# Kernel optimization log

Hardware: AMD Instinct MI355X
Metric: run time of the kernel (lower is better)

## Reference

```python
import jax, jax.numpy as jnp
import numpy as np

B, L, F, E, D, N_OUT, FC = 2048, 100, 64, 256, 256, 3, 128


def _lstm_cell(x, h, c, Wi, Wh, b):
    gates = x @ Wi + h @ Wh + b  # (B, 4H)
    i, f, g, o = jnp.split(gates, 4, axis=-1)
    c_new = jax.nn.sigmoid(f) * c + jax.nn.sigmoid(i) * jnp.tanh(g)
    h_new = jax.nn.sigmoid(o) * jnp.tanh(c_new)
    return h_new, c_new


def setup_inputs() -> dict:
    key = jax.random.key(0)
    ks = jax.random.split(key, 12)
    s = 0.05
    return {
        "x": jax.random.normal(ks[0], (B, L, F), jnp.float32),
        # encoder input-attention (shared across timesteps, as in [layer]*look_back)
        "Wa": jax.random.normal(ks[1], (F + E, F), jnp.float32) * s,
        "ba": jnp.zeros((F,), jnp.float32),
        # encoder LSTM cell
        "Wi": jax.random.normal(ks[2], (F, 4 * E), jnp.float32) * s,
        "Wh": jax.random.normal(ks[3], (E, 4 * E), jnp.float32) * s,
        "be": jnp.zeros((4 * E,), jnp.float32),
        # decoder temporal attention
        "Wd": jax.random.normal(ks[4], (E + D, D), jnp.float32) * s,
        "bd": jnp.zeros((D,), jnp.float32),
        "Wl": jax.random.normal(ks[5], (D, 1), jnp.float32) * s,
        "bl": jnp.zeros((1,), jnp.float32),
        # decoder LSTM cell
        "Wdi": jax.random.normal(ks[6], (E, 4 * D), jnp.float32) * s,
        "Wdh": jax.random.normal(ks[7], (D, 4 * D), jnp.float32) * s,
        "bdec": jnp.zeros((4 * D,), jnp.float32),
        # output head: tanh(D->FC) then tanh(FC->1)
        "Wf": jax.random.normal(ks[8], (D, FC), jnp.float32) * s,
        "bf": jnp.zeros((FC,), jnp.float32),
        "Wo": jax.random.normal(ks[9], (FC, 1), jnp.float32) * s,
        "bo": jnp.zeros((1,), jnp.float32),
    }


def reference(x, Wa, ba, Wi, Wh, be, Wd, bd, Wl, bl, Wdi, Wdh, bdec, Wf, bf, Wo, bo):
    # ---------- encoder: per-timestep input attention + LSTM cell ----------
    x_t = jnp.transpose(x, (1, 0, 2))  # (L, B, F)

    def enc_step(carry, xt):
        h, c = carry
        energies = jnp.tanh(jnp.concatenate([xt, h], axis=1) @ Wa + ba)  # (B, F)
        a = jax.nn.softmax(energies, axis=1)
        enc_in = a * xt  # attended input (B, F)
        h, c = _lstm_cell(enc_in, h, c, Wi, Wh, be)
        return (h, c), h

    h0 = jnp.zeros((B, E), x.dtype)
    c0 = jnp.zeros((B, E), x.dtype)
    _, enc_out = jax.lax.scan(enc_step, (h0, c0), x_t)  # (L, B, E)

    # ---------- decoder: temporal attention over encoder states + LSTM ----------
    h_d = jnp.zeros((B, D), x.dtype)
    c_d = jnp.zeros((B, D), x.dtype)
    outs = []
    for _ in range(N_OUT):  # small fixed output horizon
        con = jnp.broadcast_to(h_d[None, :, :], (L, B, D))
        en = jnp.tanh(jnp.concatenate([enc_out, con], axis=2) @ Wd + bd)  # (L, B, D)
        scores = en @ Wl + bl  # (L, B, 1)
        alpha = jax.nn.softmax(scores, axis=0)  # over time
        ctx = jnp.sum(alpha * enc_out, axis=0)  # (B, E)
        h_d, c_d = _lstm_cell(ctx, h_d, c_d, Wdi, Wdh, bdec)
        fc = jnp.tanh(h_d @ Wf + bf)  # (B, FC)
        outs.append(jnp.tanh(fc @ Wo + bo))  # (B, 1)
    return jnp.concatenate(outs, axis=1)  # (B, n_output)
```

## Files before the change

### kernel.cpp

```cpp
#include <hip/hip_runtime.h>
#include <math.h>

#define BB 2048
#define LL 100
#define FF 64
#define EE 256
#define DD 256
#define NOUT 3

#define COMP(v, i) ((i) == 0 ? (v).x : (i) == 1 ? (v).y : (i) == 2 ? (v).z : (v).w)

typedef unsigned short u16;
typedef unsigned int u32;
typedef __attribute__((ext_vector_type(8))) __bf16 bf16x8;
typedef __attribute__((ext_vector_type(4))) float f32x4;
typedef __attribute__((ext_vector_type(2))) float f32x2;

#define MFMA_(A, B, C) __builtin_amdgcn_mfma_f32_16x16x32_bf16((A), (B), (C), 0, 0, 0)

__device__ __forceinline__ float sigmoidf_(float x) {
    return 1.0f / (1.0f + expf(-x));
}
__device__ __forceinline__ float tanhf_(float x) {
    return 1.0f - 2.0f / (1.0f + expf(2.0f * x));
}
__device__ __forceinline__ u16 f2b_(float f) {
    u32 u = __float_as_uint(f);
    u = (u + 0x7FFFu + ((u >> 16) & 1u)) >> 16;
    return (u16)u;
}
__device__ __forceinline__ float b2f_(u16 b) {
    return __uint_as_float(((u32)b) << 16);
}
__device__ __forceinline__ u32 pack2_(float a, float b) {
    return (u32)f2b_(a) | ((u32)f2b_(b) << 16);
}
__device__ __forceinline__ f32x4 splat4(float b) {
    f32x4 v; v[0] = b; v[1] = b; v[2] = b; v[3] = b; return v;
}
__device__ __forceinline__ void split8(const float* v, uint4& H, uint4& L) {
    u16 h[8], lo[8];
    #pragma unroll
    for (int e = 0; e < 8; ++e) {
        h[e]  = f2b_(v[e]);
        lo[e] = f2b_(v[e] - b2f_(h[e]));
    }
    H = make_uint4((u32)h[0]  | ((u32)h[1]  << 16), (u32)h[2]  | ((u32)h[3]  << 16),
                   (u32)h[4]  | ((u32)h[5]  << 16), (u32)h[6]  | ((u32)h[7]  << 16));
    L = make_uint4((u32)lo[0] | ((u32)lo[1] << 16), (u32)lo[2] | ((u32)lo[3] << 16),
                   (u32)lo[4] | ((u32)lo[5] << 16), (u32)lo[6] | ((u32)lo[7] << 16));
}

#define AF(mt, kt, p, ln) (((((mt) * 10 + (kt)) * 2 + (p)) * 64 + (ln)) * 8)
#define AFX(mt, kt, p, ln) AF(mt, kt, p, (ln) ^ (((ln) >> 4) & 3))
#define AF2(mt, kt, p, ln) (((((mt) * 8 + (kt)) * 2 + (p)) * 64 + (ln)) * 8)

__global__ __launch_bounds__(64) void w_prep_all(
    const float* __restrict__ Wi, const float* __restrict__ Wh,
    const float* __restrict__ Wa, const float* __restrict__ Wd,
    u16* __restrict__ wp)
{
    const int bid = blockIdx.x;
    const int l   = threadIdx.x;

    float v[8];
    if (bid < 640) {
        const int nt = bid / 10, kt = bid - nt * 10;
        const int col = nt * 16 + (l & 15);
        #pragma unroll
        for (int e = 0; e < 8; ++e) {
            const int k = kt * 32 + ((l >> 4) << 3) + e;
            v[e] = (k < 64) ? Wi[(size_t)k * 1024 + col]
                            : Wh[(size_t)(k - 64) * 1024 + col];
        }
    } else if (bid < 680) {
        const int b2 = bid - 640;
        const int nt = b2 / 10, kt = b2 - nt * 10;
        const int col = nt * 16 + (l & 15);
        #pragma unroll
        for (int e = 0; e < 8; ++e) {
            const int k = kt * 32 + ((l >> 4) << 3) + e;
            v[e] = Wa[(size_t)k * 64 + col];
        }
    } else {
        const int b2 = bid - 680;
        const int nt = b2 >> 3, kt = b2 & 7;
        const int col = nt * 16 + (l & 15);
        #pragma unroll
        for (int e = 0; e < 8; ++e) {
            const int k = kt * 32 + ((l >> 4) << 3) + e;
            v[e] = Wd[(size_t)k * 256 + col];
        }
    }
    uint4 H, L;
    split8(v, H, L);
    *(uint4*)&wp[(size_t)bid * 1024 + (size_t)l * 8]       = H;
    *(uint4*)&wp[(size_t)bid * 1024 + 512 + (size_t)l * 8] = L;
}

__global__ __launch_bounds__(1024) void enc_mfma4(
    const float* __restrict__ x,
    const float* __restrict__ ba, const float* __restrict__ be,
    const u16* __restrict__ wp,
    float* __restrict__ enc_out,
    float* __restrict__ hbuf,
    u32* __restrict__ flags)
{
    __shared__ u16   aFrag[20480];
    __shared__ float x_s[32 * 68];
    __shared__ float e_s[32 * 68];
    __shared__ float gate_s[4][32][66];

    const int bid = blockIdx.x;
    const int g   = (bid & 7) | ((bid >> 5) << 3);
    const int p   = (bid >> 3) & 3;
    const int row0 = g * 32;
    const int tid = threadIdx.x;
    const int l   = tid & 63;
    const int w   = tid >> 6;

    for (int v = tid; v < 20480 / 2; v += 1024) ((u32*)aFrag)[v] = 0u;

    const int ntW = (w >> 2) * 16 + p * 4 + (w & 3);
    uint4 BhR[10];
    #pragma unroll
    for (int kt = 0; kt < 10; ++kt)
        BhR[kt] = *(const uint4*)&wp[(size_t)(ntW * 10 + kt) * 1024 + (size_t)l * 8];

    const float be_r = be[(size_t)ntW * 16 + (l & 15)];
    const float ba_r = (w < 8) ? ba[(w & 3) * 16 + (l & 15)] : 0.f;

    float c_state[2] = {0.f, 0.f};

    __syncthreads();

    for (int t = 0; t < LL; ++t) {
        if (t > 0) {
            if (tid == 0) {
                const u32 target = 4u * (u32)t;
                int guard = 0;
                while (__hip_atomic_load(&flags[g * 32], __ATOMIC_RELAXED,
                                         __HIP_MEMORY_SCOPE_AGENT) < target) {
                    __builtin_amdgcn_s_sleep(1);
                    if (++guard > 2000000) break;
                }
            }
            __syncthreads();
        }

        if (tid < 256) {
            const int kt2 = tid >> 7;
            const int mt  = (tid >> 6) & 1;
            const int l2  = tid & 63;
            const int row2 = mt * 16 + (l2 & 15);
            const int f0   = kt2 * 32 + ((l2 >> 4) << 3);
            const float* xp = x + (size_t)(row0 + row2) * (LL * FF) + (size_t)t * FF + f0;
            float4 xa = *(const float4*)xp;
            float4 xb = *(const float4*)(xp + 4);
            float v[8] = {xa.x, xa.y, xa.z, xa.w, xb.x, xb.y, xb.z, xb.w};
            uint4 H, L;
            split8(v, H, L);
            *(uint4*)&aFrag[AFX(mt, kt2, 0, l2)] = H;
            *(uint4*)&aFrag[AFX(mt, kt2, 1, l2)] = L;
            *(float4*)&x_s[row2 * 68 + f0]     = xa;
            *(float4*)&x_s[row2 * 68 + f0 + 4] = xb;
        } else if (t > 0) {
            const int v   = tid - 256;
            const int prl = v >> 8;
            const int vv  = v & 255;
            const int row = vv >> 3;
            const int i8  = vv & 7;
            const int ugp = (p + 1 + prl) & 3;
            const int u8  = ugp * 64 + i8 * 8;
            const float* hp_g = hbuf + ((size_t)((t - 1) & 1) * BB + row0 + row) * 256 + u8;
            f32x4 a4, b4;
            asm volatile("global_load_dwordx4 %0, %2, off sc0 sc1\n\t"
                         "global_load_dwordx4 %1, %3, off sc0 sc1\n\t"
                         "s_waitcnt vmcnt(0)"
                         : "=v"(a4), "=v"(b4)
                         : "v"(hp_g), "v"(hp_g + 4) : "memory");
            float v8[8] = {a4[0], a4[1], a4[2], a4[3], b4[0], b4[1], b4[2], b4[3]};
            uint4 H, L;
            split8(v8, H, L);
            const int mt = row >> 4, rowT = row & 15;
            const int kt_h = 2 + (u8 >> 5);
            const int g2   = (u8 & 31) >> 3;
            const int ln   = rowT + (g2 << 4);
            *(uint4*)&aFrag[AFX(mt, kt_h, 0, ln)] = H;
            *(uint4*)&aFrag[AFX(mt, kt_h, 1, ln)] = L;
        }
        __syncthreads();

        if (w < 8) {
            const int mt  = w >> 2;
            const int nta = w & 3;
            f32x4 ea = splat4(ba_r);
            #pragma unroll
            for (int kt = 0; kt < 10; ++kt) {
                bf16x8 Ah = *(const bf16x8*)&aFrag[AFX(mt, kt, 0, l)];
                bf16x8 Al = *(const bf16x8*)&aFrag[AFX(mt, kt, 1, l)];
                const size_t o = (size_t)(640 + nta * 10 + kt) * 1024 + (size_t)l * 8;
                bf16x8 Bh = *(const bf16x8*)&wp[o];
                bf16x8 Bl = *(const bf16x8*)&wp[o + 512];
                ea = MFMA_(Ah, Bh, ea);
                ea = MFMA_(Al, Bh, ea);
                ea = MFMA_(Ah, Bl, ea);
            }
            const int colA = nta * 16 + (l & 15);
            #pragma unroll
            for (int r = 0; r < 4; ++r) {
                const int rowT = ((l >> 4) << 2) + r;
                e_s[(mt * 16 + rowT) * 68 + colA] = tanhf_(ea[r]);
            }
        }
        __syncthreads();

        if (tid < 512) {
            const int row2 = tid >> 4;
            const int c4   = (tid & 15) * 4;
            float4 ev = *(const float4*)&e_s[row2 * 68 + c4];
            float m = fmaxf(fmaxf(ev.x, ev.y), fmaxf(ev.z, ev.w));
            #pragma unroll
            for (int msk = 8; msk >= 1; msk >>= 1) m = fmaxf(m, __shfl_xor(m, msk, 64));
            float4 ex;
            ex.x = expf(ev.x - m); ex.y = expf(ev.y - m);
            ex.z = expf(ev.z - m); ex.w = expf(ev.w - m);
            float s = ex.x + ex.y + ex.z + ex.w;
            #pragma unroll
            for (int msk = 8; msk >= 1; msk >>= 1) s += __shfl_xor(s, msk, 64);
            const float inv = 1.f / s;
            float4 xv = *(const float4*)&x_s[row2 * 68 + c4];
            float ein[4] = { ex.x * inv * xv.x, ex.y * inv * xv.y,
                             ex.z * inv * xv.z, ex.w * inv * xv.w };
            const int mt   = row2 >> 4;
            const int rowT = row2 & 15;
            const int kt   = c4 >> 5;
            const int g2   = (c4 & 31) >> 3;
            const int e0   = c4 & 7;
            const int ln   = rowT + (g2 << 4);
            ushort4 h4, l4;
            #pragma unroll
            for (int e = 0; e < 4; ++e) {
                u16 hh = f2b_(ein[e]);
                u16 ll = f2b_(ein[e] - b2f_(hh));
                if (e == 0) { h4.x = hh; l4.x = ll; } else if (e == 1) { h4.y = hh; l4.y = ll; }
                else if (e == 2) { h4.z = hh; l4.z = ll; } else { h4.w = hh; l4.w = ll; }
            }
            *(ushort4*)&aFrag[AFX(mt, kt, 0, ln) + e0] = h4;
            *(ushort4*)&aFrag[AFX(mt, kt, 1, ln) + e0] = l4;
        }
        __syncthreads();

        f32x4 acc0 = splat4(be_r), acc1 = splat4(be_r);
        #pragma unroll
        for (int kt = 0; kt < 10; ++kt) {
            bf16x8 Ah0 = *(const bf16x8*)&aFrag[AFX(0, kt, 0, l)];
            bf16x8 Al0 = *(const bf16x8*)&aFrag[AFX(0, kt, 1, l)];
            bf16x8 Ah1 = *(const bf16x8*)&aFrag[AFX(1, kt, 0, l)];
            bf16x8 Al1 = *(const bf16x8*)&aFrag[AFX(1, kt, 1, l)];
            bf16x8 Bl  = *(const bf16x8*)&wp[(size_t)(ntW * 10 + kt) * 1024 + 512 + (size_t)l * 8];
            bf16x8 Bh  = __builtin_bit_cast(bf16x8, BhR[kt]);
            acc0 = MFMA_(Ah0, Bh, acc0);
            acc1 = MFMA_(Ah1, Bh, acc1);
            acc0 = MFMA_(Al0, Bh, acc0);
            acc1 = MFMA_(Al1, Bh, acc1);
            acc0 = MFMA_(Ah0, Bl, acc0);
            acc1 = MFMA_(Ah1, Bl, acc1);
        }
        {
            const int gate = w >> 2;
            const int ulb  = (w & 3) * 16 + (l & 15);
            #pragma unroll
            for (int r = 0; r < 4; ++r) {
                const int rT = ((l >> 4) << 2) + r;
                gate_s[gate][rT][ulb]      = acc0[r];
                gate_s[gate][16 + rT][ulb] = acc1[r];
            }
        }
        __syncthreads();

        {
            const int row = tid >> 5;
            const int q2  = (tid & 31) * 2;
            float gi0 = gate_s[0][row][q2], gi1 = gate_s[0][row][q2 + 1];
            float gf0 = gate_s[1][row][q2], gf1 = gate_s[1][row][q2 + 1];
            float gg0 = gate_s[2][row][q2], gg1 = gate_s[2][row][q2 + 1];
            float go0 = gate_s[3][row][q2], go1 = gate_s[3][row][q2 + 1];
            float cv0 = sigmoidf_(gf0) * c_state[0] + sigmoidf_(gi0) * tanhf_(gg0);
            float cv1 = sigmoidf_(gf1) * c_state[1] + sigmoidf_(gi1) * tanhf_(gg1);
            c_state[0] = cv0; c_state[1] = cv1;
            float hv0 = sigmoidf_(go0) * tanhf_(cv0);
            float hv1 = sigmoidf_(go1) * tanhf_(cv1);
            const int u_g = p * 64 + q2;
            *(float2*)&enc_out[((size_t)t * BB + row0 + row) * 256 + u_g]
                = make_float2(hv0, hv1);
            float* hp_g = hbuf + ((size_t)(t & 1) * BB + row0 + row) * 256 + u_g;
            f32x2 hv2; hv2[0] = hv0; hv2[1] = hv1;
            asm volatile("global_store_dwordx2 %0, %1, off sc0 sc1"
                         :: "v"(hp_g), "v"(hv2) : "memory");
            const int mt = row >> 4, rowT = row & 15;
            const int kt_h = 2 + (u_g >> 5);
            const int g2   = (u_g & 31) >> 3;
            const int ln   = rowT + (g2 << 4);
            const int e    = u_g & 7;
            ((u32*)aFrag)[(AFX(mt, kt_h, 0, ln) + e) >> 1] = pack2_(hv0, hv1);
            u16 h0 = f2b_(hv0), h1 = f2b_(hv1);
            ((u32*)aFrag)[(AFX(mt, kt_h, 1, ln) + e) >> 1] =
                (u32)f2b_(hv0 - b2f_(h0)) | ((u32)f2b_(hv1 - b2f_(h1)) << 16);
        }
        asm volatile("s_waitcnt vmcnt(0)" ::: "memory");
        __syncthreads();
        if (tid == 0)
            __hip_atomic_fetch_add(&flags[g * 32], 1u, __ATOMIC_RELEASE,
                                   __HIP_MEMORY_SCOPE_AGENT);
    }
}

__global__ __launch_bounds__(256) void gemm_ep_mfma(
    const float* __restrict__ A, const u16* __restrict__ wp,
    float* __restrict__ C)
{
    __shared__ u16   aF[2 * 8 * 2 * 64 * 8];
    __shared__ float c_s[32 * 260];
    const int m0  = blockIdx.x * 32;
    const int tid = threadIdx.x;
    const int l   = tid & 63;
    const int w   = tid >> 6;

    for (int s = tid; s < 1024; s += 256) {
        const int mt = s >> 9, kt = (s >> 6) & 7, l2 = s & 63;
        const int row2 = mt * 16 + (l2 & 15);
        const int k0   = kt * 32 + ((l2 >> 4) << 3);
        const float* ap = A + (size_t)(m0 + row2) * 256 + k0;
        float4 xa = *(const float4*)ap;
        float4 xb = *(const float4*)(ap + 4);
        float v[8] = {xa.x, xa.y, xa.z, xa.w, xb.x, xb.y, xb.z, xb.w};
        uint4 H, L;
        split8(v, H, L);
        *(uint4*)&aF[AF2(mt, kt, 0, l2)] = H;
        *(uint4*)&aF[AF2(mt, kt, 1, l2)] = L;
    }
    __syncthreads();

    f32x4 acc[2][4];
    #pragma unroll
    for (int mt = 0; mt < 2; ++mt)
        #pragma unroll
        for (int j = 0; j < 4; ++j) acc[mt][j] = splat4(0.f);

    #pragma unroll
    for (int kt = 0; kt < 8; ++kt) {
        bf16x8 Ah0 = *(const bf16x8*)&aF[AF2(0, kt, 0, l)];
        bf16x8 Al0 = *(const bf16x8*)&aF[AF2(0, kt, 1, l)];
        bf16x8 Ah1 = *(const bf16x8*)&aF[AF2(1, kt, 0, l)];
        bf16x8 Al1 = *(const bf16x8*)&aF[AF2(1, kt, 1, l)];
        #pragma unroll
        for (int j = 0; j < 4; ++j) {
            const int nt = w * 4 + j;
            const u16* bt = wp + (size_t)(680 + nt * 8 + kt) * 1024 + (size_t)l * 8;
            bf16x8 Bh = *(const bf16x8*)bt;
            bf16x8 Bl = *(const bf16x8*)(bt + 512);
            acc[0][j] = MFMA_(Ah0, Bh, acc[0][j]);
            acc[1][j] = MFMA_(Ah1, Bh, acc[1][j]);
            acc[0][j] = MFMA_(Al0, Bh, acc[0][j]);
            acc[1][j] = MFMA_(Al1, Bh, acc[1][j]);
            acc[0][j] = MFMA_(Ah0, Bl, acc[0][j]);
            acc[1][j] = MFMA_(Ah1, Bl, acc[1][j]);
        }
    }

    #pragma unroll
    for (int mt = 0; mt < 2; ++mt)
        #pragma unroll
        for (int j = 0; j < 4; ++j) {
            const int col = (w * 4 + j) * 16 + (l & 15);
            #pragma unroll
            for (int r = 0; r < 4; ++r) {
                const int row = mt * 16 + ((l >> 4) << 2) + r;
                c_s[row * 260 + col] = acc[mt][j][r];
            }
        }
    __syncthreads();
    for (int v = tid; v < 32 * 64; v += 256) {
        const int row = v >> 6, c4 = (v & 63) << 2;
        *(float4*)&C[(size_t)(m0 + row) * 256 + c4] = *(const float4*)&c_s[row * 260 + c4];
    }
}

__global__ __launch_bounds__(256) void gemm_nk256(
    const float* __restrict__ A, const float* __restrict__ W,
    const float* __restrict__ bias, float* __restrict__ C, int skip_gemm)
{
    __shared__ float a_s[32 * 256];
    const int m0   = blockIdx.x * 32;
    const int tid  = threadIdx.x;
    const int lane = tid & 63;
    const int rg   = tid >> 6;
    const int n0   = lane * 4;

    float4 bias4 = make_float4(0.f, 0.f, 0.f, 0.f);
    if (bias) bias4 = *(const float4*)&bias[n0];

    if (skip_gemm) {
        #pragma unroll
        for (int r = 0; r < 8; ++r)
            *(float4*)&C[(size_t)(m0 + rg * 8 + r) * 256 + n0] = bias4;
        return;
    }

    for (int v = tid; v < 32 * 64; v += 256)
        ((float4*)a_s)[v] = ((const float4*)(A + (size_t)m0 * 256))[v];
    __syncthreads();

    float4 acc[8];
    #pragma unroll
    for (int r = 0; r < 8; ++r) acc[r] = bias4;

    #pragma unroll 2
    for (int k = 0; k < 256; k += 4) {
        float4 wv[4];
        #pragma unroll
        for (int kk = 0; kk < 4; ++kk)
            wv[kk] = *(const float4*)&W[(size_t)(k + kk) * 256 + n0];
        float4 av[8];
        #pragma unroll
        for (int r = 0; r < 8; ++r)
            av[r] = *(const float4*)&a_s[(rg * 8 + r) * 256 + k];
        #pragma unroll
        for (int kk = 0; kk < 4; ++kk) {
            #pragma unroll
            for (int r = 0; r < 8; ++r) {
                float e = COMP(av[r], kk);
                acc[r].x += e * wv[kk].x; acc[r].y += e * wv[kk].y;
                acc[r].z += e * wv[kk].z; acc[r].w += e * wv[kk].w;
            }
        }
    }
    #pragma unroll
    for (int r = 0; r < 8; ++r)
        *(float4*)&C[(size_t)(m0 + rg * 8 + r) * 256 + n0] = acc[r];
}

__global__ __launch_bounds__(256) void pack_ep(
    float* A, const float* __restrict__ W, u16* epOut, int packed)
{
    __shared__ float a_s[32 * 256];
    const int m0   = blockIdx.x * 32;
    const int tid  = threadIdx.x;
    const int lane = tid & 63;
    const int rg   = tid >> 6;
    const int n0   = lane * 4;

    for (int v = tid; v < 32 * 64; v += 256)
        ((float4*)a_s)[v] = ((const float4*)(A + (size_t)m0 * 256))[v];
    __syncthreads();

    float4 acc[8];
    #pragma unroll
    for (int r = 0; r < 8; ++r) acc[r] = make_float4(0.f, 0.f, 0.f, 0.f);

    #pragma unroll 2
    for (int k = 0; k < 256; k += 4) {
        float4 wv[4];
        #pragma unroll
        for (int kk = 0; kk < 4; ++kk)
            wv[kk] = *(const float4*)&W[(size_t)(k + kk) * 256 + n0];
        float4 av[8];
        #pragma unroll
        for (int r = 0; r < 8; ++r)
            av[r] = *(const float4*)&a_s[(rg * 8 + r) * 256 + k];
        #pragma unroll
        for (int kk = 0; kk < 4; ++kk) {
            #pragma unroll
            for (int r = 0; r < 8; ++r) {
                float e = COMP(av[r], kk);
                acc[r].x += e * wv[kk].x; acc[r].y += e * wv[kk].y;
                acc[r].z += e * wv[kk].z; acc[r].w += e * wv[kk].w;
            }
        }
    }

    u16* epu = packed ? (u16*)A : epOut;
    #pragma unroll
    for (int r = 0; r < 8; ++r) {
        const size_t row = (size_t)(m0 + rg * 8 + r);
        ushort4 o;
        o.x = f2b_(acc[r].x); o.y = f2b_(acc[r].y);
        o.z = f2b_(acc[r].z); o.w = f2b_(acc[r].w);
        u16* dst = packed ? (epu + row * 512 + 256 + n0)
                          : (epu + row * 256 + n0);
        *(ushort4*)dst = o;
    }

    if (packed) {
        u32* ab = (u32*)A;
        for (int v = tid; v < 32 * 128; v += 256) {
            const int row = v >> 7, j = v & 127;
            float2 f = *(const float2*)&a_s[(row << 8) + (j << 1)];
            ab[((size_t)(m0 + row)) * 256 + j] = pack2_(f.x, f.y);
        }
    }
}

__global__ __launch_bounds__(256) void scores_ep_f32(
    const float* __restrict__ ep, const float* __restrict__ hp,
    const float* __restrict__ Wl, float* __restrict__ scores)
{
    __shared__ float hp_s[8 * 256];
    const int b0  = blockIdx.x * 8;
    const int l0  = blockIdx.y * 20;
    const int tid = threadIdx.x;
    const int r   = tid >> 5;
    const int g   = tid & 31;

    for (int v = tid; v < 512; v += 256)
        ((float4*)hp_s)[v] = ((const float4*)(hp + (size_t)b0 * 256))[v];
    __syncthreads();

    const float4 wl0 = *(const float4*)&Wl[g * 4];
    const float4 wl1 = *(const float4*)&Wl[128 + g * 4];
    const float4 h0  = *(const float4*)&hp_s[r * 256 + g * 4];
    const float4 h1  = *(const float4*)&hp_s[r * 256 + 128 + g * 4];
    const float* eb  = ep + (size_t)l0 * (BB * 256) + (size_t)(b0 + r) * 256;

    #pragma unroll 2
    for (int li = 0; li < 20; ++li) {
        float4 e0 = *(const float4*)&eb[(size_t)li * (BB * 256) + g * 4];
        float4 e1 = *(const float4*)&eb[(size_t)li * (BB * 256) + 128 + g * 4];
        float p = tanhf_(e0.x + h0.x) * wl0.x + tanhf_(e0.y + h0.y) * wl0.y
                + tanhf_(e0.z + h0.z) * wl0.z + tanhf_(e0.w + h0.w) * wl0.w
                + tanhf_(e1.x + h1.x) * wl1.x + tanhf_(e1.y + h1.y) * wl1.y
                + tanhf_(e1.z + h1.z) * wl1.z + tanhf_(e1.w + h1.w) * wl1.w;
        #pragma unroll
        for (int msk = 16; msk >= 1; msk >>= 1) p += __shfl_xor(p, msk, 64);
        if (g == 0) scores[(size_t)(l0 + li) * BB + b0 + r] = p;
    }
}

__global__ __launch_bounds__(256) void scores_ep_b16(
    const u16* __restrict__ ep, const float* __restrict__ hp,
    const float* __restrict__ Wl, float* __restrict__ scores,
    int sstr, int soff)
{
    __shared__ float hp_s[8 * 256];
    const int b0  = blockIdx.x * 8;
    const int l0  = blockIdx.y * 20;
    const int tid = threadIdx.x;
    const int r   = tid >> 5;
    const int g   = tid & 31;

    for (int v = tid; v < 512; v += 256)
        ((float4*)hp_s)[v] = ((const float4*)(hp + (size_t)b0 * 256))[v];
    __syncthreads();

    const float4 wl0 = *(const float4*)&Wl[g * 4];
    const float4 wl1 = *(const float4*)&Wl[128 + g * 4];
    const float4 h0  = *(const float4*)&hp_s[r * 256 + g * 4];
    const float4 h1  = *(const float4*)&hp_s[r * 256 + 128 + g * 4];

    #pragma unroll 2
    for (int li = 0; li < 20; ++li) {
        const u16* er = ep + ((size_t)(l0 + li) * BB + b0 + r) * sstr + soff;
        ushort4 u0 = *(const ushort4*)&er[g * 4];
        ushort4 u1 = *(const ushort4*)&er[128 + g * 4];
        float p = tanhf_(b2f_(u0.x) + h0.x) * wl0.x + tanhf_(b2f_(u0.y) + h0.y) * wl0.y
                + tanhf_(b2f_(u0.z) + h0.z) * wl0.z + tanhf_(b2f_(u0.w) + h0.w) * wl0.w
                + tanhf_(b2f_(u1.x) + h1.x) * wl1.x + tanhf_(b2f_(u1.y) + h1.y) * wl1.y
                + tanhf_(b2f_(u1.z) + h1.z) * wl1.z + tanhf_(b2f_(u1.w) + h1.w) * wl1.w;
        #pragma unroll
        for (int msk = 16; msk >= 1; msk >>= 1) p += __shfl_xor(p, msk, 64);
        if (g == 0) scores[(size_t)(l0 + li) * BB + b0 + r] = p;
    }
}

__global__ __launch_bounds__(256) void softmax_ctx(
    const float* __restrict__ scores, const float* __restrict__ enc_out,
    float* __restrict__ ctx)
{
    __shared__ float al_s[8 * 100];
    const int b0  = blockIdx.x * 8;
    const int tid = threadIdx.x;
    for (int v = tid; v < 800; v += 256) {
        int r = v / 100, l = v - r * 100;
        al_s[r * 100 + l] = scores[(size_t)l * BB + b0 + r];
    }
    __syncthreads();
    if (tid < 8) {
        float m = -1e30f;
        for (int l = 0; l < LL; ++l) m = fmaxf(m, al_s[tid * 100 + l]);
        float s = 0.f;
        for (int l = 0; l < LL; ++l) { float e = expf(al_s[tid * 100 + l] - m); al_s[tid * 100 + l] = e; s += e; }
        float inv = 1.f / s;
        for (int l = 0; l < LL; ++l) al_s[tid * 100 + l] *= inv;
    }
    __syncthreads();
    float acc[8] = {};
    for (int l = 0; l < LL; ++l) {
        const float* er = enc_out + (size_t)l * (BB * 256) + (size_t)b0 * 256 + tid;
        #pragma unroll
        for (int r = 0; r < 8; ++r) acc[r] += al_s[r * 100 + l] * er[r * 256];
    }
    for (int r = 0; r < 8; ++r) ctx[(size_t)(b0 + r) * 256 + tid] = acc[r];
}

__global__ __launch_bounds__(256) void softmax_ctx_b16(
    const float* __restrict__ scores, const u16* __restrict__ encp,
    float* __restrict__ ctx)
{
    __shared__ float al_s[8 * 100];
    const int b0  = blockIdx.x * 8;
    const int tid = threadIdx.x;
    for (int v = tid; v < 800; v += 256) {
        int r = v / 100, l = v - r * 100;
        al_s[r * 100 + l] = scores[(size_t)l * BB + b0 + r];
    }
    __syncthreads();
    if (tid < 8) {
        float m = -1e30f;
        for (int l = 0; l < LL; ++l) m = fmaxf(m, al_s[tid * 100 + l]);
        float s = 0.f;
        for (int l = 0; l < LL; ++l) { float e = expf(al_s[tid * 100 + l] - m); al_s[tid * 100 + l] = e; s += e; }
        float inv = 1.f / s;
        for (int l = 0; l < LL; ++l) al_s[tid * 100 + l] *= inv;
    }
    __syncthreads();
    float acc[8] = {};
    for (int l = 0; l < LL; ++l) {
        const u16* er = encp + ((size_t)l * BB + b0) * 512 + tid;
        #pragma unroll
        for (int r = 0; r < 8; ++r) acc[r] += al_s[r * 100 + l] * b2f_(er[r * 512]);
    }
    for (int r = 0; r < 8; ++r) ctx[(size_t)(b0 + r) * 256 + tid] = acc[r];
}

__global__ __launch_bounds__(512) void dec_step(
    const float* __restrict__ ctxp,
    const float* __restrict__ Wdi, const float* __restrict__ Wdh,
    const float* __restrict__ bdec,
    float* __restrict__ hd, float* __restrict__ c_st, int first)
{
    __shared__ float ct_s[8 * 256];
    __shared__ float hd_s[8 * 256];
    __shared__ float gate_s[2][8 * 1024];
    const int row0 = blockIdx.x * 8;
    const int tid  = threadIdx.x;
    const int lane = tid & 63, w = tid >> 6;
    const int half = tid >> 8;
    const int ct   = tid & 255;
    const int c0   = ct * 4;

    ((float4*)ct_s)[tid] = ((const float4*)(ctxp + (size_t)row0 * 256))[tid];
    if (!first)
        ((float4*)hd_s)[tid] = ((const float4*)(hd + (size_t)row0 * 256))[tid];
    __syncthreads();

    float4 acc[8];
    {
        float4 b4 = *(const float4*)&bdec[c0];
        float4 bias4 = (half == 0) ? b4 : make_float4(0.f, 0.f, 0.f, 0.f);
        #pragma unroll
        for (int r = 0; r < 8; ++r) acc[r] = bias4;
    }
    if (half == 0) {
        const float* wP = Wdi + c0;
        #pragma unroll 2
        for (int ch = 0; ch < 64; ++ch) {
            const int k0 = ch * 4;
            float4 w0 = *(const float4*)&wP[(size_t)(k0 + 0) * 1024];
            float4 w1 = *(const float4*)&wP[(size_t)(k0 + 1) * 1024];
            float4 w2 = *(const float4*)&wP[(size_t)(k0 + 2) * 1024];
            float4 w3 = *(const float4*)&wP[(size_t)(k0 + 3) * 1024];
            #pragma unroll
            for (int r = 0; r < 8; ++r) {
                float4 av = *(const float4*)&ct_s[r * 256 + k0];
                acc[r].x += av.x * w0.x; acc[r].y += av.x * w0.y;
                acc[r].z += av.x * w0.z; acc[r].w += av.x * w0.w;
                acc[r].x += av.y * w1.x; acc[r].y += av.y * w1.y;
                acc[r].z += av.y * w1.z; acc[r].w += av.y * w1.w;
                acc[r].x += av.z * w2.x; acc[r].y += av.z * w2.y;
                acc[r].z += av.z * w2.z; acc[r].w += av.z * w2.w;
                acc[r].x += av.w * w3.x; acc[r].y += av.w * w3.y;
                acc[r].z += av.w * w3.z; acc[r].w += av.w * w3.w;
            }
        }
    } else if (!first) {
        const float* wP = Wdh + c0;
        #pragma unroll 2
        for (int ch = 0; ch < 64; ++ch) {
            const int k0 = ch * 4;
            float4 w0 = *(const float4*)&wP[(size_t)(k0 + 0) * 1024];
            float4 w1 = *(const float4*)&wP[(size_t)(k0 + 1) * 1024];
            float4 w2 = *(const float4*)&wP[(size_t)(k0 + 2) * 1024];
            float4 w3 = *(const float4*)&wP[(size_t)(k0 + 3) * 1024];
            #pragma unroll
            for (int r = 0; r < 8; ++r) {
                float4 av = *(const float4*)&hd_s[r * 256 + k0];
                acc[r].x += av.x * w0.x; acc[r].y += av.x * w0.y;
                acc[r].z += av.x * w0.z; acc[r].w += av.x * w0.w;
                acc[r].x += av.y * w1.x; acc[r].y += av.y * w1.y;
                acc[r].z += av.y * w1.z; acc[r].w += av.y * w1.w;
                acc[r].x += av.z * w2.x; acc[r].y += av.z * w2.y;
                acc[r].z += av.z * w2.z; acc[r].w += av.z * w2.w;
                acc[r].x += av.w * w3.x; acc[r].y += av.w * w3.y;
                acc[r].z += av.w * w3.z; acc[r].w += av.w * w3.w;
            }
        }
    }
    #pragma unroll
    for (int r = 0; r < 8; ++r)
        *(float4*)&gate_s[half][r * 1024 + c0] = acc[r];
    __syncthreads();

    {
        const float* g0 = &gate_s[0][w * 1024 + lane * 4];
        const float* g1 = &gate_s[1][w * 1024 + lane * 4];
        float4 giA = *(const float4*)&g0[0],   giB = *(const float4*)&g1[0];
        float4 gfA = *(const float4*)&g0[256], gfB = *(const float4*)&g1[256];
        float4 ggA = *(const float4*)&g0[512], ggB = *(const float4*)&g1[512];
        float4 goA = *(const float4*)&g0[768], goB = *(const float4*)&g1[768];
        size_t ci = (size_t)(row0 + w) * 256 + lane * 4;
        float4 c4 = first ? make_float4(0.f, 0.f, 0.f, 0.f)
                          : *(const float4*)&c_st[ci];
        float cc[4] = { c4.x, c4.y, c4.z, c4.w };
        float gi[4] = { giA.x + giB.x, giA.y + giB.y, giA.z + giB.z, giA.w + giB.w };
        float gf[4] = { gfA.x + gfB.x, gfA.y + gfB.y, gfA.z + gfB.z, gfA.w + gfB.w };
        float gg[4] = { ggA.x + ggB.x, ggA.y + ggB.y, ggA.z + ggB.z, ggA.w + ggB.w };
        float go[4] = { goA.x + goB.x, goA.y + goB.y, goA.z + goB.z, goA.w + goB.w };
        float4 cn, hn;
        #pragma unroll
        for (int uu = 0; uu < 4; ++uu) {
            float cv = sigmoidf_(gf[uu]) * cc[uu] + sigmoidf_(gi[uu]) * tanhf_(gg[uu]);
            float hv = sigmoidf_(go[uu]) * tanhf_(cv);
            if (uu == 0) { cn.x = cv; hn.x = hv; } else if (uu == 1) { cn.y = cv; hn.y = hv; }
            else if (uu == 2) { cn.z = cv; hn.z = hv; } else { cn.w = cv; hn.w = hv; }
        }
        *(float4*)&c_st[ci] = cn;
        *(float4*)&hd[ci]   = hn;
    }
}

__global__ __launch_bounds__(256) void head_k(
    const float* __restrict__ hd, const float* __restrict__ Wf,
    const float* __restrict__ bf, const float* __restrict__ Wo,
    const float* __restrict__ bo, float* __restrict__ out, int step)
{
    __shared__ float hd_s[16 * 256];
    __shared__ float fc_s[16 * 128];
    const int b0  = blockIdx.x * 16;
    const int tid = threadIdx.x;
    {
        const float4* hg = (const float4*)(hd + (size_t)b0 * 256);
        for (int i = tid; i < 1024; i += 256) ((float4*)hd_s)[i] = hg[i];
    }
    __syncthreads();
    {
        const int f = tid & 127, rg = tid >> 7;
        float acc[8];
        float bfv = bf[f];
        #pragma unroll
        for (int rr = 0; rr < 8; ++rr) acc[rr] = bfv;
        const float* wp = Wf + f;
        #pragma unroll 2
        for (int k = 0; k < 256; ++k) {
            float wv = wp[k * 128];
            #pragma unroll
            for (int rr = 0; rr < 8; ++rr) acc[rr] += hd_s[(rg * 8 + rr) * 256 + k] * wv;
        }
        for (int rr = 0; rr < 8; ++rr) fc_s[(rg * 8 + rr) * 128 + f] = tanhf_(acc[rr]);
    }
    __syncthreads();
    {
        const int lane = tid & 63, w = tid >> 6;
        const float bov = bo[0];
        #pragma unroll
        for (int rr = 0; rr < 4; ++rr) {
            int r = w * 4 + rr;
            float p = fc_s[r * 128 + lane] * Wo[lane] + fc_s[r * 128 + 64 + lane] * Wo[64 + lane];
            #pragma unroll
            for (int msk = 32; msk >= 1; msk >>= 1) p += __shfl_xor(p, msk, 64);
            if (lane == 0) out[(size_t)(b0 + r) * NOUT + step] = tanhf_(p + bov);
        }
    }
}

extern "C" void kernel_launch(void* const* d_in, const int* in_sizes, int n_in,
                              void* d_out, int out_size, void* d_ws, size_t ws_size,
                              hipStream_t stream)
{
    const float* x    = (const float*)d_in[0];
    const float* Wa   = (const float*)d_in[1];
    const float* ba   = (const float*)d_in[2];
    const float* Wi   = (const float*)d_in[3];
    const float* Wh   = (const float*)d_in[4];
    const float* be   = (const float*)d_in[5];
    const float* Wd   = (const float*)d_in[6];
    const float* bd   = (const float*)d_in[7];
    const float* Wl   = (const float*)d_in[8];
    const float* bl   = (const float*)d_in[9];
    const float* Wdi  = (const float*)d_in[10];
    const float* Wdh  = (const float*)d_in[11];
    const float* bdec = (const float*)d_in[12];
    const float* Wf   = (const float*)d_in[13];
    const float* bf   = (const float*)d_in[14];
    const float* Wo   = (const float*)d_in[15];
    const float* bo   = (const float*)d_in[16];
    float* out = (float*)d_out;

    const size_t f_enc    = (size_t)LL * BB * EE;
    const size_t f_state  = (size_t)BB * EE;
    const size_t f_scores = (size_t)LL * BB;
    const size_t need3 = (f_enc + 3 * f_state + f_scores) * sizeof(float);
    const size_t need2 = need3 + f_enc * sizeof(u16);
    const size_t need1 = need3 + f_enc * sizeof(float);

    float* ws      = (float*)d_ws;
    float* enc_out = ws;
    float* hd      = enc_out + f_enc;
    float* c_d     = hd + f_state;
    float* ctx     = c_d + f_state;
    float* scores  = ctx + f_state;
    float* ep32    = scores + f_scores;
    u16*   ep16    = (u16*)(scores + f_scores);
    float* hp      = ctx;
    u16*   wprep   = (u16*)ctx;
    float* hbuf    = hd;
    u32*   flags   = (u32*)scores;

    if (ws_size < need3) return;
    const int tier = (ws_size >= need1) ? 1 : (ws_size >= need2) ? 2 : 3;

    hipMemsetAsync(flags, 0, 64 * 32 * sizeof(u32), stream);
    w_prep_all<<<808, 64, 0, stream>>>(Wi, Wh, Wa, Wd, wprep);
    enc_mfma4<<<256, 1024, 0, stream>>>(x, ba, be, wprep, enc_out, hbuf, flags);

    if (tier == 1)
        gemm_ep_mfma<<<(LL * BB) / 32, 256, 0, stream>>>(enc_out, wprep, ep32);
    else
        pack_ep<<<(LL * BB) / 32, 256, 0, stream>>>(
            enc_out, Wd, ep16, tier == 3 ? 1 : 0);

    for (int s = 0; s < NOUT; ++s) {
        gemm_nk256<<<BB / 32, 256, 0, stream>>>(
            hd, Wd + 256 * 256, bd, hp, s == 0);
        if (tier == 1)
            scores_ep_f32<<<dim3(BB / 8, 5), 256, 0, stream>>>(ep32, hp, Wl, scores);
        else if (tier == 2)
            scores_ep_b16<<<dim3(BB / 8, 5), 256, 0, stream>>>(ep16, hp, Wl, scores, 256, 0);
        else
            scores_ep_b16<<<dim3(BB / 8, 5), 256, 0, stream>>>(
                (const u16*)enc_out, hp, Wl, scores, 512, 256);
        if (tier == 3)
            softmax_ctx_b16<<<BB / 8, 256, 0, stream>>>(scores, (const u16*)enc_out, ctx);
        else
            softmax_ctx<<<BB / 8, 256, 0, stream>>>(scores, enc_out, ctx);
        dec_step<<<BB / 8, 512, 0, stream>>>(ctx, Wdi, Wdh, bdec, hd, c_d, s == 0);
        head_k<<<BB / 16, 256, 0, stream>>>(hd, Wf, bf, Wo, bo, out, s);
    }
}
```

Before: 2.251 ms.

## Overlap encoder recurrent GEMM with attention phases and fuse decoder scores-softmax-context

In the encoder step, the h-dependent part of the LSTM gate GEMM (k-tiles 2..9) now runs during the attention-energy and softmax phases. Idle warps take it on in each phase, so only the x-dependent k-tiles remain after the last barrier. The softmax now runs on warps 8+ instead of the first 512 threads. Separately, the tier-1 decoder path fuses score computation, softmax over time and context reduction into one kernel. This removes a launch and the scores round trip, but the fused kernel uses fewer blocks and does a serial per-row softmax on 8 threads.

```diff
diff --git a/kernel.cpp b/kernel.cpp
--- a/kernel.cpp
+++ b/kernel.cpp
@@ -191,6 +191,8 @@
         }
         __syncthreads();
 
+        f32x4 acc0, acc1;
+
         if (w < 8) {
             const int mt  = w >> 2;
             const int nta = w & 3;
@@ -212,12 +214,30 @@
                 const int rowT = ((l >> 4) << 2) + r;
                 e_s[(mt * 16 + rowT) * 68 + colA] = tanhf_(ea[r]);
             }
+        } else {
+            acc0 = splat4(be_r); acc1 = splat4(be_r);
+            #pragma unroll
+            for (int kt = 2; kt < 10; ++kt) {
+                bf16x8 Ah0 = *(const bf16x8*)&aFrag[AFX(0, kt, 0, l)];
+                bf16x8 Al0 = *(const bf16x8*)&aFrag[AFX(0, kt, 1, l)];
+                bf16x8 Ah1 = *(const bf16x8*)&aFrag[AFX(1, kt, 0, l)];
+                bf16x8 Al1 = *(const bf16x8*)&aFrag[AFX(1, kt, 1, l)];
+                bf16x8 Bl  = *(const bf16x8*)&wp[(size_t)(ntW * 10 + kt) * 1024 + 512 + (size_t)l * 8];
+                bf16x8 Bh  = __builtin_bit_cast(bf16x8, BhR[kt]);
+                acc0 = MFMA_(Ah0, Bh, acc0);
+                acc1 = MFMA_(Ah1, Bh, acc1);
+                acc0 = MFMA_(Al0, Bh, acc0);
+                acc1 = MFMA_(Al1, Bh, acc1);
+                acc0 = MFMA_(Ah0, Bl, acc0);
+                acc1 = MFMA_(Ah1, Bl, acc1);
+            }
         }
         __syncthreads();
 
-        if (tid < 512) {
-            const int row2 = tid >> 4;
-            const int c4   = (tid & 15) * 4;
+        if (w >= 8) {
+            const int v2   = tid - 512;
+            const int row2 = v2 >> 4;
+            const int c4   = (v2 & 15) * 4;
             float4 ev = *(const float4*)&e_s[row2 * 68 + c4];
             float m = fmaxf(fmaxf(ev.x, ev.y), fmaxf(ev.z, ev.w));
             #pragma unroll
@@ -248,12 +268,28 @@
             }
             *(ushort4*)&aFrag[AFX(mt, kt, 0, ln) + e0] = h4;
             *(ushort4*)&aFrag[AFX(mt, kt, 1, ln) + e0] = l4;
+        } else {
+            acc0 = splat4(be_r); acc1 = splat4(be_r);
+            #pragma unroll
+            for (int kt = 2; kt < 10; ++kt) {
+                bf16x8 Ah0 = *(const bf16x8*)&aFrag[AFX(0, kt, 0, l)];
+                bf16x8 Al0 = *(const bf16x8*)&aFrag[AFX(0, kt, 1, l)];
+                bf16x8 Ah1 = *(const bf16x8*)&aFrag[AFX(1, kt, 0, l)];
+                bf16x8 Al1 = *(const bf16x8*)&aFrag[AFX(1, kt, 1, l)];
+                bf16x8 Bl  = *(const bf16x8*)&wp[(size_t)(ntW * 10 + kt) * 1024 + 512 + (size_t)l * 8];
+                bf16x8 Bh  = __builtin_bit_cast(bf16x8, BhR[kt]);
+                acc0 = MFMA_(Ah0, Bh, acc0);
+                acc1 = MFMA_(Ah1, Bh, acc1);
+                acc0 = MFMA_(Al0, Bh, acc0);
+                acc1 = MFMA_(Al1, Bh, acc1);
+                acc0 = MFMA_(Ah0, Bl, acc0);
+                acc1 = MFMA_(Ah1, Bl, acc1);
+            }
         }
         __syncthreads();
 
-        f32x4 acc0 = splat4(be_r), acc1 = splat4(be_r);
-        #pragma unroll
-        for (int kt = 0; kt < 10; ++kt) {
+        #pragma unroll
+        for (int kt = 0; kt < 2; ++kt) {
             bf16x8 Ah0 = *(const bf16x8*)&aFrag[AFX(0, kt, 0, l)];
             bf16x8 Al0 = *(const bf16x8*)&aFrag[AFX(0, kt, 1, l)];
             bf16x8 Ah1 = *(const bf16x8*)&aFrag[AFX(1, kt, 0, l)];
@@ -502,38 +538,59 @@
     }
 }
 
-__global__ __launch_bounds__(256) void scores_ep_f32(
+__global__ __launch_bounds__(512) void scores_sm_ctx(
     const float* __restrict__ ep, const float* __restrict__ hp,
-    const float* __restrict__ Wl, float* __restrict__ scores)
+    const float* __restrict__ Wl, const float* __restrict__ enc_out,
+    float* __restrict__ ctx)
 {
     __shared__ float hp_s[8 * 256];
+    __shared__ float al_s[8 * 100];
     const int b0  = blockIdx.x * 8;
-    const int l0  = blockIdx.y * 20;
     const int tid = threadIdx.x;
-    const int r   = tid >> 5;
-    const int g   = tid & 31;
-
-    for (int v = tid; v < 512; v += 256)
+
+    for (int v = tid; v < 512; v += 512)
         ((float4*)hp_s)[v] = ((const float4*)(hp + (size_t)b0 * 256))[v];
     __syncthreads();
 
-    const float4 wl0 = *(const float4*)&Wl[g * 4];
-    const float4 wl1 = *(const float4*)&Wl[128 + g * 4];
-    const float4 h0  = *(const float4*)&hp_s[r * 256 + g * 4];
-    const float4 h1  = *(const float4*)&hp_s[r * 256 + 128 + g * 4];
-    const float* eb  = ep + (size_t)l0 * (BB * 256) + (size_t)(b0 + r) * 256;
-
-    #pragma unroll 2
-    for (int li = 0; li < 20; ++li) {
-        float4 e0 = *(const float4*)&eb[(size_t)li * (BB * 256) + g * 4];
-        float4 e1 = *(const float4*)&eb[(size_t)li * (BB * 256) + 128 + g * 4];
-        float p = tanhf_(e0.x + h0.x) * wl0.x + tanhf_(e0.y + h0.y) * wl0.y
-                + tanhf_(e0.z + h0.z) * wl0.z + tanhf_(e0.w + h0.w) * wl0.w
-                + tanhf_(e1.x + h1.x) * wl1.x + tanhf_(e1.y + h1.y) * wl1.y
-                + tanhf_(e1.z + h1.z) * wl1.z + tanhf_(e1.w + h1.w) * wl1.w;
-        #pragma unroll
-        for (int msk = 16; msk >= 1; msk >>= 1) p += __shfl_xor(p, msk, 64);
-        if (g == 0) scores[(size_t)(l0 + li) * BB + b0 + r] = p;
+    {
+        const int r = tid >> 6;
+        const int g = tid & 63;
+        const float4 wl4 = *(const float4*)&Wl[g * 4];
+        const float4 h4  = *(const float4*)&hp_s[r * 256 + g * 4];
+        for (int l = 0; l < LL; ++l) {
+            const float* er = ep + ((size_t)l * BB + b0 + r) * 256;
+            float4 e4 = *(const float4*)&er[g * 4];
+            float p = tanhf_(e4.x + h4.x) * wl4.x + tanhf_(e4.y + h4.y) * wl4.y
+                    + tanhf_(e4.z + h4.z) * wl4.z + tanhf_(e4.w + h4.w) * wl4.w;
+            #pragma unroll
+            for (int msk = 32; msk >= 1; msk >>= 1) p += __shfl_xor(p, msk, 64);
+            if (g == 0) al_s[r * 100 + l] = p;
+        }
+    }
+    __syncthreads();
+    if (tid < 8) {
+        float m = -1e30f;
+        for (int l = 0; l < LL; ++l) m = fmaxf(m, al_s[tid * 100 + l]);
+        float s = 0.f;
+        for (int l = 0; l < LL; ++l) { float e = expf(al_s[tid * 100 + l] - m); al_s[tid * 100 + l] = e; s += e; }
+        float inv = 1.f / s;
+        for (int l = 0; l < LL; ++l) al_s[tid * 100 + l] *= inv;
+    }
+    __syncthreads();
+    {
+        const int u  = tid & 255;
+        const int rh = tid >> 8;
+        float acc[4] = {};
+        for (int l = 0; l < LL; ++l) {
+            const float* er2 = enc_out + (size_t)l * (BB * 256)
+                             + (size_t)(b0 + rh * 4) * 256 + u;
+            #pragma unroll
+            for (int j = 0; j < 4; ++j)
+                acc[j] += al_s[(rh * 4 + j) * 100 + l] * er2[j * 256];
+        }
+        #pragma unroll
+        for (int j = 0; j < 4; ++j)
+            ctx[(size_t)(b0 + rh * 4 + j) * 256 + u] = acc[j];
     }
 }
 
@@ -842,17 +899,16 @@
     for (int s = 0; s < NOUT; ++s) {
         gemm_nk256<<<BB / 32, 256, 0, stream>>>(
             hd, Wd + 256 * 256, bd, hp, s == 0);
-        if (tier == 1)
-            scores_ep_f32<<<dim3(BB / 8, 5), 256, 0, stream>>>(ep32, hp, Wl, scores);
-        else if (tier == 2)
+        if (tier == 1) {
+            scores_sm_ctx<<<BB / 8, 512, 0, stream>>>(ep32, hp, Wl, enc_out, ctx);
+        } else if (tier == 2) {
             scores_ep_b16<<<dim3(BB / 8, 5), 256, 0, stream>>>(ep16, hp, Wl, scores, 256, 0);
-        else
+            softmax_ctx<<<BB / 8, 256, 0, stream>>>(scores, enc_out, ctx);
+        } else {
             scores_ep_b16<<<dim3(BB / 8, 5), 256, 0, stream>>>(
                 (const u16*)enc_out, hp, Wl, scores, 512, 256);
-        if (tier == 3)
             softmax_ctx_b16<<<BB / 8, 256, 0, stream>>>(scores, (const u16*)enc_out, ctx);
-        else
-            softmax_ctx<<<BB / 8, 256, 0, stream>>>(scores, enc_out, ctx);
+        }
         dec_step<<<BB / 8, 512, 0, stream>>>(ctx, Wdi, Wdh, bdec, hd, c_d, s == 0);
         head_k<<<BB / 16, 256, 0, stream>>>(hd, Wf, bf, Wo, bo, out, s);
     }
```

After: 2.249 ms. About the same (-0.1%).
